# Kernel tuning notes

Measured on AMD Instinct MI355X. Metric: run time of the kernel, lower is better.

The kernel has to match this reference:

```python
import jax, jax.numpy as jnp
import numpy as np

H = 1024      # hidden_size
NH = 16       # num_heads
HD = H // NH  # head_dim


def setup_inputs() -> dict:
    key = jax.random.key(0)
    ks = jax.random.split(key, 12)
    inp = {
        "query": jax.random.normal(ks[0], (4, 1024, H), dtype=jnp.float32),
        "key": jax.random.normal(ks[1], (4, 2048, H), dtype=jnp.float32),
        "value": jax.random.normal(ks[2], (4, 2048, H), dtype=jnp.float32),
        "key_padding_mask": jax.random.randint(ks[3], (4, 2048), 0, 2, dtype=jnp.int32),
        # learned parameters (torch Linear: y = x @ W.T + b); we store W already transposed
        "Wq": jax.random.normal(ks[4], (H, H), dtype=jnp.float32) * (1.0 / np.sqrt(H)),
        "bq": jnp.zeros((H,), dtype=jnp.float32),
        "Wk": jax.random.normal(ks[5], (H, H), dtype=jnp.float32) * (1.0 / np.sqrt(H)),
        "bk": jnp.zeros((H,), dtype=jnp.float32),
        "Wv": jax.random.normal(ks[6], (H, H), dtype=jnp.float32) * (1.0 / np.sqrt(H)),
        "bv": jnp.zeros((H,), dtype=jnp.float32),
        "Wo": jax.random.normal(ks[7], (H, H), dtype=jnp.float32) * (1.0 / np.sqrt(H)),
        "bo": jnp.zeros((H,), dtype=jnp.float32),
    }
    return inp


def reference(query, key, value, key_padding_mask, Wq, bq, Wk, bk, Wv, bv, Wo, bo):
    B, Sq, _ = query.shape
    Sk = key.shape[1]
    scaling = HD ** -0.5
    # projections -> [B, NH, S, HD]
    q = (query @ Wq + bq).reshape(B, Sq, NH, HD).transpose(0, 2, 1, 3)
    k = (key @ Wk + bk).reshape(B, Sk, NH, HD).transpose(0, 2, 1, 3)
    v = (value @ Wv + bv).reshape(B, Sk, NH, HD).transpose(0, 2, 1, 3)
    # scores [B, NH, Sq, Sk]
    scores = jnp.einsum("bhqd,bhkd->bhqk", q, k) * scaling
    # mask: positions where key_padding_mask == 0 are ignored
    scores = jnp.where((key_padding_mask == 0)[:, None, None, :], -jnp.inf, scores)
    attn = jax.nn.softmax(scores, axis=-1)
    # dropout is identity in eval mode
    out = jnp.einsum("bhqk,bhkd->bhqd", attn, v)
    out = out.transpose(0, 2, 1, 3).reshape(B, Sq, H)
    return out @ Wo + bo
```

## Files before the change

### kernel.cpp

```cpp
#include <hip/hip_runtime.h>
#include <hip/hip_fp16.h>
#include <math.h>

#define B_ 4
#define SQ 1024
#define SK 2048
#define HH 1024
#define NHEAD 16
#define HDIM 64

typedef _Float16 f16;
typedef __attribute__((ext_vector_type(8))) _Float16 f16x8;
typedef __attribute__((ext_vector_type(4))) _Float16 f16x4;
typedef __attribute__((ext_vector_type(4))) float f32x4;
typedef unsigned int u32;

#define GLOAD_LDS16(gp, lp) __builtin_amdgcn_global_load_lds( \
    (const __attribute__((address_space(1))) u32*)(gp),        \
    (__attribute__((address_space(3))) u32*)(lp), 16, 0, 0)
#define GLOAD_LDS4(gp, lp) __builtin_amdgcn_global_load_lds(  \
    (const __attribute__((address_space(1))) u32*)(gp),        \
    (__attribute__((address_space(3))) u32*)(lp), 4, 0, 0)

__global__ __launch_bounds__(256) void prep_k(
    const float* __restrict__ q, const float* __restrict__ k,
    const float* __restrict__ v,
    const float* __restrict__ W0, const float* __restrict__ W1,
    const float* __restrict__ W2, const float* __restrict__ W3,
    const int* __restrict__ mask,
    f16* __restrict__ qo, f16* __restrict__ ko, f16* __restrict__ vo,
    f16* __restrict__ WT, float* __restrict__ pbias)
{
    __shared__ f16 t[64 * 80];
    const int bid = blockIdx.x, tid = threadIdx.x;
    if (bid < 10240) {
        int i = bid * 256 + tid;
        const float* src; f16* dst; int j;
        if (i < 524288)       { src = q; dst = qo; j = i; }
        else if (i < 1572864) { src = k; dst = ko; j = i - 524288; }
        else                  { src = v; dst = vo; j = i - 1572864; }
        float4 a = ((const float4*)src)[(size_t)j * 2];
        float4 b = ((const float4*)src)[(size_t)j * 2 + 1];
        f16x8 o;
        o[0] = (f16)a.x; o[1] = (f16)a.y; o[2] = (f16)a.z; o[3] = (f16)a.w;
        o[4] = (f16)b.x; o[5] = (f16)b.y; o[6] = (f16)b.z; o[7] = (f16)b.w;
        *(f16x8*)(dst + (size_t)j * 8) = o;
    } else if (bid < 11264) {
        int id = bid - 10240;
        int z = id >> 8, idx = id & 255;
        const float* W = z == 0 ? W0 : z == 1 ? W1 : z == 2 ? W2 : W3;
        f16* out = WT + (size_t)z * HH * HH;
        const int r0 = (idx >> 4) * 64, c0 = (idx & 15) * 64;
#pragma unroll
        for (int p = 0; p < 4; p++) {
            int s = p * 256 + tid;
            int row = s >> 4, u = s & 15;
            float4 a = *(const float4*)(W + (size_t)(r0 + row) * HH + c0 + u * 4);
            f16x4 vv;
            vv[0] = (f16)a.x; vv[1] = (f16)a.y; vv[2] = (f16)a.z; vv[3] = (f16)a.w;
            *(f16x4*)(t + row * 80 + u * 4) = vv;
        }
        __syncthreads();
#pragma unroll
        for (int p = 0; p < 2; p++) {
            int s = p * 256 + tid;
            int n = s >> 3, u = s & 7;
            f16x8 vv;
#pragma unroll
            for (int j = 0; j < 8; j++) vv[j] = t[(u * 8 + j) * 80 + n];
            *(f16x8*)(out + (size_t)(c0 + n) * HH + r0 + u * 8) = vv;
        }
    } else {
        int j = (bid - 11264) * 256 + tid;
        pbias[j] = mask[j] ? 0.f : -1e30f;
    }
}

template <int TM, int OUTMODE>
__device__ __forceinline__ void gemm_body(
    const f16* __restrict__ A, const f16* __restrict__ BT,
    const float* __restrict__ bias, void* __restrict__ Cout,
    int M, int bid, int nwg, f16* sA, f16* sB)
{
    const int tid = threadIdx.x, lane = tid & 63, w = tid >> 6;
    const int swz = (bid & 7) * (nwg >> 3) + (bid >> 3);
    const int m0 = (swz >> 3) * TM;
    const int n0 = (swz & 7) * 128;
    const int wr = w >> 1, wc = w & 1;
    const int ql = lane & 15, g = lane >> 4;
    const int N = 1024, K = 1024;
    const int MF = TM / 32;
    const int ABUF = TM * 32;
    f32x4 acc[TM / 32][4] = {};

    auto stage = [&](int buf, int k0) {
#pragma unroll
        for (int p = 0; p < TM / 64; p++) {
            int s = p * 256 + tid;
            int row = s >> 2, us = ((s & 3) ^ ((row >> 1) & 3)) * 8;
            GLOAD_LDS16(A + (size_t)(m0 + row) * K + k0 + us,
                        sA + buf * ABUF + (p * 256 + w * 64) * 8);
        }
#pragma unroll
        for (int p = 0; p < 2; p++) {
            int s = p * 256 + tid;
            int row = s >> 2, us = ((s & 3) ^ ((row >> 1) & 3)) * 8;
            GLOAD_LDS16(BT + (size_t)(n0 + row) * K + k0 + us,
                        sB + buf * 4096 + (p * 256 + w * 64) * 8);
        }
    };

    stage(0, 0);
    int cur = 0;
    for (int k0 = 0; k0 < K; k0 += 32) {
        __syncthreads();
        if (k0 + 32 < K) stage(cur ^ 1, k0 + 32);
        f16x8 af[MF], bf[4];
#pragma unroll
        for (int m = 0; m < MF; m++) {
            int row = wr * (TM / 2) + m * 16 + ql;
            af[m] = *(const f16x8*)(sA + cur * ABUF + row * 32 + ((g ^ ((row >> 1) & 3)) * 8));
        }
#pragma unroll
        for (int n = 0; n < 4; n++) {
            int row = wc * 64 + n * 16 + ql;
            bf[n] = *(const f16x8*)(sB + cur * 4096 + row * 32 + ((g ^ ((row >> 1) & 3)) * 8));
        }
#pragma unroll
        for (int m = 0; m < MF; m++)
#pragma unroll
            for (int n = 0; n < 4; n++)
                acc[m][n] = __builtin_amdgcn_mfma_f32_16x16x32_f16(af[m], bf[n], acc[m][n], 0, 0, 0);
        cur ^= 1;
    }

    float bv[4];
#pragma unroll
    for (int n = 0; n < 4; n++) bv[n] = bias[n0 + wc * 64 + n * 16 + ql];
#pragma unroll
    for (int m = 0; m < MF; m++) {
        int row0 = m0 + wr * (TM / 2) + m * 16 + g * 4;
#pragma unroll
        for (int n = 0; n < 4; n++) {
            int col = n0 + wc * 64 + n * 16 + ql;
            if (OUTMODE == 2) {
                int bb = row0 >> 11, kk = row0 & 2047;
                int hh = col >> 6, dd = col & 63;
                f16x4 vv;
#pragma unroll
                for (int e = 0; e < 4; e++) vv[e] = (f16)(acc[m][n][e] + bv[n]);
                *(f16x4*)((f16*)Cout + ((size_t)(bb * NHEAD + hh) * HDIM + dd) * SK + kk) = vv;
            } else if (OUTMODE == 1) {
#pragma unroll
                for (int e = 0; e < 4; e++)
                    ((f16*)Cout)[(size_t)(row0 + e) * N + col] = (f16)(acc[m][n][e] + bv[n]);
            } else {
#pragma unroll
                for (int e = 0; e < 4; e++)
                    ((float*)Cout)[(size_t)(row0 + e) * N + col] = acc[m][n][e] + bv[n];
            }
        }
    }
}

__global__ __launch_bounds__(256) void qkv_gemm_k(
    const f16* __restrict__ qc, const f16* __restrict__ kc,
    const f16* __restrict__ vc, const f16* __restrict__ wT,
    const float* __restrict__ bq, const float* __restrict__ bk,
    const float* __restrict__ bv,
    f16* __restrict__ qp, f16* __restrict__ kp, f16* __restrict__ vt)
{
    __shared__ f16 sA[2 * 4096];
    __shared__ f16 sB[2 * 4096];
    const int bid = blockIdx.x;
    const size_t M1 = 1024 * 1024;
    if (bid < 512)
        gemm_body<64, 1>(qc, wT, bq, qp, 4096, bid, 512, sA, sB);
    else if (bid < 1024)
        gemm_body<128, 1>(kc, wT + M1, bk, kp, 8192, bid - 512, 512, sA, sB);
    else
        gemm_body<128, 2>(vc, wT + 2 * M1, bv, vt, 8192, bid - 1024, 512, sA, sB);
}

__global__ __launch_bounds__(256) void o_gemm_k(
    const f16* __restrict__ ctx, const f16* __restrict__ wT,
    const float* __restrict__ bo, float* __restrict__ out)
{
    __shared__ f16 sA[2 * 4096];
    __shared__ f16 sB[2 * 4096];
    gemm_body<64, 0>(ctx, wT, bo, out, 4096, blockIdx.x, 512, sA, sB);
}

#define SC2 0.18033688f
#define THR2 11.5f

__global__ __launch_bounds__(512, 6) void attn_mfma_k(
    const f16* __restrict__ qp,
    const f16* __restrict__ kp,
    const f16* __restrict__ vt,
    const float* __restrict__ pbias,
    f16* __restrict__ ctx)
{
    const int flat = ((int)blockIdx.x & 7) * 64 + ((int)blockIdx.x >> 3);
    const int qt = flat & 7, h = (flat >> 3) & 15, b = flat >> 7;
    const int q0 = qt * 128;
    const int tid = threadIdx.x, lane = tid & 63, w = tid >> 6;
    const int ql = lane & 15, g = lane >> 4;

    __shared__ f16 ks[2 * 4096];
    __shared__ f16 vs[2 * 4096];
    __shared__ f16 plds[8][16 * 80];
    __shared__ float sbias[2][64];

    const f16* kbase = kp + (size_t)b * SK * HH + h * HDIM;
    const f16* vbase = vt + ((size_t)(b * NHEAD + h)) * HDIM * SK;
    const float* bbase = pbias + b * SK;

    f16x8 qf[2];
    {
        const f16* qb = qp + ((size_t)(b * SQ + q0 + w * 16 + ql)) * HH + h * HDIM + g * 8;
        qf[0] = *(const f16x8*)qb;
        qf[1] = *(const f16x8*)(qb + 32);
    }

    auto stageKV = [&](int buf, int kt) {
        int r = tid >> 3, ulg = ((tid & 7) ^ (r & 7)) * 8;
        GLOAD_LDS16(kbase + (size_t)(kt + r) * HH + ulg, ks + buf * 4096 + w * 512);
        GLOAD_LDS16(vbase + (size_t)r * SK + kt + ulg,   vs + buf * 4096 + w * 512);
        if (w == 0) GLOAD_LDS4(bbase + kt + lane, &sbias[buf][0]);
    };

    f32x4 oacc[4] = {};
    float mrun = -1e30f, lrun = 0.f;

    stageKV(0, 0);
    int cur = 0;
    for (int kt = 0; kt < SK; kt += 64) {
        __syncthreads();
        if (kt + 64 < SK) stageKV(cur ^ 1, kt + 64);
        const f16* kb = ks + cur * 4096;
        const f16* vb = vs + cur * 4096;

        f32x4 sacc[4] = {};
        __builtin_amdgcn_s_setprio(1);
#pragma unroll
        for (int n = 0; n < 4; n++) {
            int key = n * 16 + ql;
#pragma unroll
            for (int df = 0; df < 2; df++) {
                int u = df * 4 + g;
                f16x8 kf = *(const f16x8*)(kb + key * 64 + ((u ^ (key & 7)) * 8));
                sacc[n] = __builtin_amdgcn_mfma_f32_16x16x32_f16(kf, qf[df], sacc[n], 0, 0, 0);
            }
        }
        __builtin_amdgcn_s_setprio(0);

        float sv[4][4];
        float mt = -1e30f;
#pragma unroll
        for (int n = 0; n < 4; n++) {
            float4 b4 = *(const float4*)&sbias[cur][n * 16 + g * 4];
            float barr[4] = {b4.x, b4.y, b4.z, b4.w};
#pragma unroll
            for (int e = 0; e < 4; e++) {
                float s = fmaf(sacc[n][e], SC2, barr[e]);
                sv[n][e] = s;
                mt = fmaxf(mt, s);
            }
        }
        mt = fmaxf(mt, __shfl_xor(mt, 16, 64));
        mt = fmaxf(mt, __shfl_xor(mt, 32, 64));

        if (__any(mt > mrun + THR2)) {
            float mnew = fmaxf(mrun, mt);
            float alpha = __builtin_amdgcn_exp2f(mrun - mnew);
            mrun = mnew;
            lrun *= alpha;
            float al[4];
#pragma unroll
            for (int e = 0; e < 4; e++) al[e] = __shfl(alpha, g * 4 + e, 64);
#pragma unroll
            for (int df = 0; df < 4; df++)
#pragma unroll
                for (int e = 0; e < 4; e++) oacc[df][e] *= al[e];
        }

        float tsum = 0.f;
#pragma unroll
        for (int n = 0; n < 4; n++) {
            float p0 = __builtin_amdgcn_exp2f(sv[n][0] - mrun);
            float p1 = __builtin_amdgcn_exp2f(sv[n][1] - mrun);
            float p2 = __builtin_amdgcn_exp2f(sv[n][2] - mrun);
            float p3 = __builtin_amdgcn_exp2f(sv[n][3] - mrun);
            tsum += (p0 + p1) + (p2 + p3);
            f16x4 pv4;
            pv4[0] = (f16)p0; pv4[1] = (f16)p1; pv4[2] = (f16)p2; pv4[3] = (f16)p3;
            *(f16x4*)(plds[w] + ql * 80 + n * 16 + g * 4) = pv4;
        }
        tsum += __shfl_xor(tsum, 16, 64);
        tsum += __shfl_xor(tsum, 32, 64);
        lrun += tsum;

        __builtin_amdgcn_s_setprio(1);
#pragma unroll
        for (int t = 0; t < 2; t++) {
            f16x8 pf = *(const f16x8*)(plds[w] + ql * 80 + t * 32 + g * 8);
#pragma unroll
            for (int df = 0; df < 4; df++) {
                int d = df * 16 + ql;
                int u = t * 4 + g;
                f16x8 vf = *(const f16x8*)(vb + d * 64 + ((u ^ (d & 7)) * 8));
                oacc[df] = __builtin_amdgcn_mfma_f32_16x16x32_f16(pf, vf, oacc[df], 0, 0, 0);
            }
        }
        __builtin_amdgcn_s_setprio(0);
        cur ^= 1;
    }

    float linv[4];
#pragma unroll
    for (int e = 0; e < 4; e++) {
        float lv = __shfl(lrun, g * 4 + e, 64);
        linv[e] = 1.f / lv;
    }
    f16* ob = ctx + ((size_t)(b * SQ + q0 + w * 16)) * HH + h * HDIM;
#pragma unroll
    for (int df = 0; df < 4; df++)
#pragma unroll
        for (int e = 0; e < 4; e++)
            ob[(size_t)(g * 4 + e) * HH + df * 16 + ql] = (f16)(oacc[df][e] * linv[e]);
}

extern "C" void kernel_launch(void* const* d_in, const int* in_sizes, int n_in,
                              void* d_out, int out_size, void* d_ws, size_t ws_size,
                              hipStream_t stream) {
    const float* query = (const float*)d_in[0];
    const float* key   = (const float*)d_in[1];
    const float* value = (const float*)d_in[2];
    const int*   mask  = (const int*)d_in[3];
    const float* Wq = (const float*)d_in[4];
    const float* bq = (const float*)d_in[5];
    const float* Wk = (const float*)d_in[6];
    const float* bk = (const float*)d_in[7];
    const float* Wv = (const float*)d_in[8];
    const float* bv = (const float*)d_in[9];
    const float* Wo = (const float*)d_in[10];
    const float* bo = (const float*)d_in[11];
    float* out = (float*)d_out;

    const size_t M1 = 1024 * 1024;
    f16* qcast = (f16*)d_ws;
    f16* kcast = qcast + 4 * M1;
    f16* vcast = kcast + 8 * M1;
    f16* wT    = vcast + 8 * M1;
    f16* qp    = wT + 4 * M1;
    f16* kp    = qp + 4 * M1;
    f16* vt    = kp + 8 * M1;
    float* pbias = (float*)(vt + 8 * M1);
    f16* ctx   = qcast;

    dim3 blk(256);

    prep_k<<<dim3(11296), blk, 0, stream>>>(query, key, value, Wq, Wk, Wv, Wo,
                                            mask, qcast, kcast, vcast, wT, pbias);

    qkv_gemm_k<<<dim3(1536), blk, 0, stream>>>(qcast, kcast, vcast, wT,
                                               bq, bk, bv, qp, kp, vt);

    attn_mfma_k<<<dim3(512), dim3(512), 0, stream>>>(qp, kp, vt, pbias, ctx);

    o_gemm_k<<<dim3(512), blk, 0, stream>>>(ctx, wT + 3 * M1, bo, out);
}
```

Baseline: 166.1 us.

## Fuse fp32-to-fp16 input cast into QKV GEMM and restructure attention loop

The separate pass that cast query/key/value to fp16 is removed. The QKV GEMM now loads fp32 activations directly, converts them in registers and writes swizzled fp16 into LDS, which drops a full read/write round trip of the activations. The attention kernel also unrolls its K/V double-buffer loop into two statically addressed tiles, replaces the padded P scratch buffer with an XOR-swizzled unpadded layout, and lowers the launch-bounds occupancy hint from 6 to 4. The fused load path gives up the asynchronous global-to-LDS copy for A in exchange for register staging, which may expose more load latency in the GEMM.

```diff
diff --git a/kernel.cpp b/kernel.cpp
--- a/kernel.cpp
+++ b/kernel.cpp
@@ -23,31 +23,15 @@
     (__attribute__((address_space(3))) u32*)(lp), 4, 0, 0)
 
 __global__ __launch_bounds__(256) void prep_k(
-    const float* __restrict__ q, const float* __restrict__ k,
-    const float* __restrict__ v,
     const float* __restrict__ W0, const float* __restrict__ W1,
     const float* __restrict__ W2, const float* __restrict__ W3,
     const int* __restrict__ mask,
-    f16* __restrict__ qo, f16* __restrict__ ko, f16* __restrict__ vo,
     f16* __restrict__ WT, float* __restrict__ pbias)
 {
     __shared__ f16 t[64 * 80];
     const int bid = blockIdx.x, tid = threadIdx.x;
-    if (bid < 10240) {
-        int i = bid * 256 + tid;
-        const float* src; f16* dst; int j;
-        if (i < 524288)       { src = q; dst = qo; j = i; }
-        else if (i < 1572864) { src = k; dst = ko; j = i - 524288; }
-        else                  { src = v; dst = vo; j = i - 1572864; }
-        float4 a = ((const float4*)src)[(size_t)j * 2];
-        float4 b = ((const float4*)src)[(size_t)j * 2 + 1];
-        f16x8 o;
-        o[0] = (f16)a.x; o[1] = (f16)a.y; o[2] = (f16)a.z; o[3] = (f16)a.w;
-        o[4] = (f16)b.x; o[5] = (f16)b.y; o[6] = (f16)b.z; o[7] = (f16)b.w;
-        *(f16x8*)(dst + (size_t)j * 8) = o;
-    } else if (bid < 11264) {
-        int id = bid - 10240;
-        int z = id >> 8, idx = id & 255;
+    if (bid < 1024) {
+        int z = bid >> 8, idx = bid & 255;
         const float* W = z == 0 ? W0 : z == 1 ? W1 : z == 2 ? W2 : W3;
         f16* out = WT + (size_t)z * HH * HH;
         const int r0 = (idx >> 4) * 64, c0 = (idx & 15) * 64;
@@ -71,16 +55,16 @@
             *(f16x8*)(out + (size_t)(c0 + n) * HH + r0 + u * 8) = vv;
         }
     } else {
-        int j = (bid - 11264) * 256 + tid;
+        int j = (bid - 1024) * 256 + tid;
         pbias[j] = mask[j] ? 0.f : -1e30f;
     }
 }
 
-template <int TM, int OUTMODE>
+template <int TM, int OUTMODE, int CASTA>
 __device__ __forceinline__ void gemm_body(
-    const f16* __restrict__ A, const f16* __restrict__ BT,
+    const void* Ain, const f16* __restrict__ BT,
     const float* __restrict__ bias, void* __restrict__ Cout,
-    int M, int bid, int nwg, f16* sA, f16* sB)
+    int bid, int nwg, f16* sA, f16* sB)
 {
     const int tid = threadIdx.x, lane = tid & 63, w = tid >> 6;
     const int swz = (bid & 7) * (nwg >> 3) + (bid >> 3);
@@ -94,12 +78,29 @@
     f32x4 acc[TM / 32][4] = {};
 
     auto stage = [&](int buf, int k0) {
-#pragma unroll
-        for (int p = 0; p < TM / 64; p++) {
-            int s = p * 256 + tid;
-            int row = s >> 2, us = ((s & 3) ^ ((row >> 1) & 3)) * 8;
-            GLOAD_LDS16(A + (size_t)(m0 + row) * K + k0 + us,
-                        sA + buf * ABUF + (p * 256 + w * 64) * 8);
+        if (CASTA) {
+            const float* A32 = (const float*)Ain;
+#pragma unroll
+            for (int p = 0; p < TM / 64; p++) {
+                int s = p * 256 + tid;
+                int row = s >> 2, u = s & 3;
+                const float* ap = A32 + (size_t)(m0 + row) * K + k0 + u * 8;
+                float4 a0 = *(const float4*)ap;
+                float4 a1 = *(const float4*)(ap + 4);
+                f16x8 v;
+                v[0] = (f16)a0.x; v[1] = (f16)a0.y; v[2] = (f16)a0.z; v[3] = (f16)a0.w;
+                v[4] = (f16)a1.x; v[5] = (f16)a1.y; v[6] = (f16)a1.z; v[7] = (f16)a1.w;
+                *(f16x8*)(sA + buf * ABUF + row * 32 + ((u ^ ((row >> 1) & 3)) * 8)) = v;
+            }
+        } else {
+            const f16* A16 = (const f16*)Ain;
+#pragma unroll
+            for (int p = 0; p < TM / 64; p++) {
+                int s = p * 256 + tid;
+                int row = s >> 2, us = ((s & 3) ^ ((row >> 1) & 3)) * 8;
+                GLOAD_LDS16(A16 + (size_t)(m0 + row) * K + k0 + us,
+                            sA + buf * ABUF + (p * 256 + w * 64) * 8);
+            }
         }
 #pragma unroll
         for (int p = 0; p < 2; p++) {
@@ -164,8 +165,8 @@
 }
 
 __global__ __launch_bounds__(256) void qkv_gemm_k(
-    const f16* __restrict__ qc, const f16* __restrict__ kc,
-    const f16* __restrict__ vc, const f16* __restrict__ wT,
+    const float* __restrict__ q, const float* __restrict__ k,
+    const float* __restrict__ v, const f16* __restrict__ wT,
     const float* __restrict__ bq, const float* __restrict__ bk,
     const float* __restrict__ bv,
     f16* __restrict__ qp, f16* __restrict__ kp, f16* __restrict__ vt)
@@ -175,11 +176,11 @@
     const int bid = blockIdx.x;
     const size_t M1 = 1024 * 1024;
     if (bid < 512)
-        gemm_body<64, 1>(qc, wT, bq, qp, 4096, bid, 512, sA, sB);
+        gemm_body<64, 1, 1>(q, wT, bq, qp, bid, 512, sA, sB);
     else if (bid < 1024)
-        gemm_body<128, 1>(kc, wT + M1, bk, kp, 8192, bid - 512, 512, sA, sB);
+        gemm_body<128, 1, 1>(k, wT + M1, bk, kp, bid - 512, 512, sA, sB);
     else
-        gemm_body<128, 2>(vc, wT + 2 * M1, bv, vt, 8192, bid - 1024, 512, sA, sB);
+        gemm_body<128, 2, 1>(v, wT + 2 * M1, bv, vt, bid - 1024, 512, sA, sB);
 }
 
 __global__ __launch_bounds__(256) void o_gemm_k(
@@ -188,13 +189,13 @@
 {
     __shared__ f16 sA[2 * 4096];
     __shared__ f16 sB[2 * 4096];
-    gemm_body<64, 0>(ctx, wT, bo, out, 4096, blockIdx.x, 512, sA, sB);
+    gemm_body<64, 0, 0>(ctx, wT, bo, out, blockIdx.x, 512, sA, sB);
 }
 
 #define SC2 0.18033688f
 #define THR2 11.5f
 
-__global__ __launch_bounds__(512, 6) void attn_mfma_k(
+__global__ __launch_bounds__(512, 4) void attn_mfma_k(
     const f16* __restrict__ qp,
     const f16* __restrict__ kp,
     const f16* __restrict__ vt,
@@ -209,7 +210,7 @@
 
     __shared__ f16 ks[2 * 4096];
     __shared__ f16 vs[2 * 4096];
-    __shared__ f16 plds[8][16 * 80];
+    __shared__ f16 plds[8][16 * 64];
     __shared__ float sbias[2][64];
 
     const f16* kbase = kp + (size_t)b * SK * HH + h * HDIM;
@@ -232,14 +233,12 @@
 
     f32x4 oacc[4] = {};
     float mrun = -1e30f, lrun = 0.f;
-
-    stageKV(0, 0);
-    int cur = 0;
-    for (int kt = 0; kt < SK; kt += 64) {
+    f16* pw = &plds[w][0];
+
+    auto tile = [&](const f16* kb, const f16* vb, const float* sb,
+                    bool pf_en, int pbuf, int pkt) {
         __syncthreads();
-        if (kt + 64 < SK) stageKV(cur ^ 1, kt + 64);
-        const f16* kb = ks + cur * 4096;
-        const f16* vb = vs + cur * 4096;
+        if (pf_en) stageKV(pbuf, pkt);
 
         f32x4 sacc[4] = {};
         __builtin_amdgcn_s_setprio(1);
@@ -259,7 +258,7 @@
         float mt = -1e30f;
 #pragma unroll
         for (int n = 0; n < 4; n++) {
-            float4 b4 = *(const float4*)&sbias[cur][n * 16 + g * 4];
+            float4 b4 = *(const float4*)&sb[n * 16 + g * 4];
             float barr[4] = {b4.x, b4.y, b4.z, b4.w};
 #pragma unroll
             for (int e = 0; e < 4; e++) {
@@ -295,7 +294,7 @@
             tsum += (p0 + p1) + (p2 + p3);
             f16x4 pv4;
             pv4[0] = (f16)p0; pv4[1] = (f16)p1; pv4[2] = (f16)p2; pv4[3] = (f16)p3;
-            *(f16x4*)(plds[w] + ql * 80 + n * 16 + g * 4) = pv4;
+            *(f16x4*)(pw + ql * 64 + (((2 * n + (g >> 1)) ^ (ql & 7)) * 8) + (g & 1) * 4) = pv4;
         }
         tsum += __shfl_xor(tsum, 16, 64);
         tsum += __shfl_xor(tsum, 32, 64);
@@ -304,7 +303,7 @@
         __builtin_amdgcn_s_setprio(1);
 #pragma unroll
         for (int t = 0; t < 2; t++) {
-            f16x8 pf = *(const f16x8*)(plds[w] + ql * 80 + t * 32 + g * 8);
+            f16x8 pf = *(const f16x8*)(pw + ql * 64 + (((t * 4 + g) ^ (ql & 7)) * 8));
 #pragma unroll
             for (int df = 0; df < 4; df++) {
                 int d = df * 16 + ql;
@@ -314,7 +313,13 @@
             }
         }
         __builtin_amdgcn_s_setprio(0);
-        cur ^= 1;
+    };
+
+    stageKV(0, 0);
+#pragma unroll 1
+    for (int kt = 0; kt < SK; kt += 128) {
+        tile(ks, vs, sbias[0], true, 1, kt + 64);
+        tile(ks + 4096, vs + 4096, sbias[1], kt + 128 < SK, 0, kt + 128);
     }
 
     float linv[4];
@@ -349,22 +354,18 @@
     float* out = (float*)d_out;
 
     const size_t M1 = 1024 * 1024;
-    f16* qcast = (f16*)d_ws;
-    f16* kcast = qcast + 4 * M1;
-    f16* vcast = kcast + 8 * M1;
-    f16* wT    = vcast + 8 * M1;
+    f16* wT    = (f16*)d_ws;
     f16* qp    = wT + 4 * M1;
     f16* kp    = qp + 4 * M1;
     f16* vt    = kp + 8 * M1;
-    float* pbias = (float*)(vt + 8 * M1);
-    f16* ctx   = qcast;
+    f16* ctx   = vt + 8 * M1;
+    float* pbias = (float*)(ctx + 4 * M1);
 
     dim3 blk(256);
 
-    prep_k<<<dim3(11296), blk, 0, stream>>>(query, key, value, Wq, Wk, Wv, Wo,
-                                            mask, qcast, kcast, vcast, wT, pbias);
-
-    qkv_gemm_k<<<dim3(1536), blk, 0, stream>>>(qcast, kcast, vcast, wT,
+    prep_k<<<dim3(1056), blk, 0, stream>>>(Wq, Wk, Wv, Wo, mask, wT, pbias);
+
+    qkv_gemm_k<<<dim3(1536), blk, 0, stream>>>(query, key, value, wT,
                                                bq, bk, bv, qp, kp, vt);
 
     attn_mfma_k<<<dim3(512), dim3(512), 0, stream>>>(qp, kp, vt, pbias, ctx);
```

After: 170.6 us. 2.7% more time.
